# Performance work log

Hardware: AMD Instinct MI355X
Metric: run time of the kernel (lower is better)

## Reference

```python
import jax, jax.numpy as jnp
import numpy as np

N_EMBD = 1024
N_HEAD = 16
HEAD = N_EMBD // N_HEAD
D_FF = 4 * N_EMBD
B, T = 2, 2048


def setup_inputs() -> dict:
    key = jax.random.key(0)
    ks = jax.random.split(key, 12)
    s = 0.02
    return {
        "x": jax.random.normal(ks[0], (B, T, N_EMBD), jnp.float32),
        "Wq": jax.random.normal(ks[1], (N_EMBD, N_EMBD), jnp.float32) * s,
        "bq": jnp.zeros((N_EMBD,), jnp.float32),
        "Wk": jax.random.normal(ks[2], (N_EMBD, N_EMBD), jnp.float32) * s,
        "bk": jnp.zeros((N_EMBD,), jnp.float32),
        "Wv": jax.random.normal(ks[3], (N_EMBD, N_EMBD), jnp.float32) * s,
        "bv": jnp.zeros((N_EMBD,), jnp.float32),
        "Wo": jax.random.normal(ks[4], (N_EMBD, N_EMBD), jnp.float32) * s,
        "bo": jnp.zeros((N_EMBD,), jnp.float32),
        "W1": jax.random.normal(ks[5], (N_EMBD, D_FF), jnp.float32) * s,
        "b1": jnp.zeros((D_FF,), jnp.float32),
        "W2": jax.random.normal(ks[6], (D_FF, N_EMBD), jnp.float32) * s,
        "b2": jnp.zeros((N_EMBD,), jnp.float32),
        "g1": jnp.ones((N_EMBD,), jnp.float32),
        "be1": jnp.zeros((N_EMBD,), jnp.float32),
        "g2": jnp.ones((N_EMBD,), jnp.float32),
        "be2": jnp.zeros((N_EMBD,), jnp.float32),
    }


def _layernorm(x, g, b, eps=1e-3):
    # keras LayerNormalization default epsilon=1e-3
    mu = jnp.mean(x, axis=-1, keepdims=True)
    var = jnp.mean(jnp.square(x - mu), axis=-1, keepdims=True)
    return (x - mu) * jax.lax.rsqrt(var + eps) * g + b


def _attention(h, Wq, bq, Wk, bk, Wv, bv, Wo, bo):
    b, t, _ = h.shape
    q = (h @ Wq + bq).reshape(b, t, N_HEAD, HEAD)
    k = (h @ Wk + bk).reshape(b, t, N_HEAD, HEAD)
    v = (h @ Wv + bv).reshape(b, t, N_HEAD, HEAD)
    scores = jnp.einsum("bthd,bshd->bhts", q, k) / jnp.sqrt(jnp.float32(HEAD))
    causal = jnp.tril(jnp.ones((t, t), bool))
    scores = jnp.where(causal, scores, -jnp.inf)
    w = jax.nn.softmax(scores, axis=-1)  # dropout is identity in eval
    ctx = jnp.einsum("bhts,bshd->bthd", w, v).reshape(b, t, N_EMBD)
    return ctx @ Wo + bo


def reference(x, Wq, bq, Wk, bk, Wv, bv, Wo, bo, W1, b1, W2, b2, g1, be1, g2, be2):
    x = x + _attention(_layernorm(x, g1, be1), Wq, bq, Wk, bk, Wv, bv, Wo, bo)
    h = _layernorm(x, g2, be2)
    ff = jax.nn.relu(h @ W1 + b1) @ W2 + b2
    return x + ff
```

## Files before the change

### kernel.cpp

```cpp
#include <hip/hip_runtime.h>

typedef __bf16 bf16;
typedef __attribute__((ext_vector_type(8))) __bf16 bf16x8;
typedef __attribute__((ext_vector_type(4))) __bf16 bf16x4;
typedef __attribute__((ext_vector_type(4))) float f32x4;

#define MFMA16(A, B, C) __builtin_amdgcn_mfma_f32_16x16x32_bf16(A, B, C, 0, 0, 0)

#define GLOAD16(gp, lp)                                          \
  __builtin_amdgcn_global_load_lds(                              \
      (const __attribute__((address_space(1))) void*)(gp),       \
      (__attribute__((address_space(3))) void*)(lp), 16, 0, 0)

__device__ __forceinline__ float fexp2(float x) {
#if __has_builtin(__builtin_amdgcn_exp2f)
  return __builtin_amdgcn_exp2f(x);
#else
  float r;
  asm("v_exp_f32 %0, %1" : "=v"(r) : "v"(x));
  return r;
#endif
}

#define QSCL 0.18033688011112042f

__global__ __launch_bounds__(256) void transpose_cvt_kernel(
    const float* __restrict__ in, bf16* __restrict__ out, int K, int N)
{
  __shared__ float tile[32][33];
  const int kt = blockIdx.y * 32;
  const int nt = blockIdx.x * 32;
  const int tx = threadIdx.x, ty = threadIdx.y;
#pragma unroll
  for (int j = 0; j < 4; ++j)
    tile[ty + j * 8][tx] = in[(size_t)(kt + ty + j * 8) * N + nt + tx];
  __syncthreads();
#pragma unroll
  for (int j = 0; j < 4; ++j)
    out[(size_t)(nt + ty + j * 8) * K + kt + tx] = (bf16)tile[tx][ty + j * 8];
}

__global__ __launch_bounds__(256) void transpose4_cvt_kernel(
    const float* __restrict__ w0, const float* __restrict__ w1,
    const float* __restrict__ w2, const float* __restrict__ w3,
    bf16* __restrict__ out)
{
  __shared__ float tile[32][33];
  const float* srcs[4] = {w0, w1, w2, w3};
  const float* in = srcs[blockIdx.z];
  bf16* o = out + (size_t)blockIdx.z * 1024 * 1024;
  const int kt = blockIdx.y * 32;
  const int nt = blockIdx.x * 32;
  const int tx = threadIdx.x, ty = threadIdx.y;
#pragma unroll
  for (int j = 0; j < 4; ++j)
    tile[ty + j * 8][tx] = in[(size_t)(kt + ty + j * 8) * 1024 + nt + tx];
  __syncthreads();
#pragma unroll
  for (int j = 0; j < 4; ++j)
    o[(size_t)(nt + ty + j * 8) * 1024 + kt + tx] = (bf16)tile[tx][ty + j * 8];
}

__global__ __launch_bounds__(256) void ln_kernel(
    const float* __restrict__ in, const float* __restrict__ gamma,
    const float* __restrict__ beta, bf16* __restrict__ out)
{
  const int row = blockIdx.x;
  const int t = threadIdx.x;
  const float4 v = ((const float4*)(in + (size_t)row * 1024))[t];
  float s = v.x + v.y + v.z + v.w;
  float sq = v.x * v.x + v.y * v.y + v.z * v.z + v.w * v.w;
#pragma unroll
  for (int m = 1; m < 64; m <<= 1) {
    s += __shfl_xor(s, m);
    sq += __shfl_xor(sq, m);
  }
  __shared__ float ssum[4], ssq[4];
  const int w = t >> 6;
  if ((t & 63) == 0) { ssum[w] = s; ssq[w] = sq; }
  __syncthreads();
  s = ssum[0] + ssum[1] + ssum[2] + ssum[3];
  sq = ssq[0] + ssq[1] + ssq[2] + ssq[3];
  const float mu = s * (1.0f / 1024.0f);
  const float var = sq * (1.0f / 1024.0f) - mu * mu;
  const float rs = rsqrtf(var + 1e-3f);
  const float4 g = ((const float4*)gamma)[t];
  const float4 b = ((const float4*)beta)[t];
  bf16x4 o;
  o[0] = (bf16)((v.x - mu) * rs * g.x + b.x);
  o[1] = (bf16)((v.y - mu) * rs * g.y + b.y);
  o[2] = (bf16)((v.z - mu) * rs * g.z + b.z);
  o[3] = (bf16)((v.w - mu) * rs * g.w + b.w);
  *(bf16x4*)(out + (size_t)row * 1024 + t * 4) = o;
}

__global__ __launch_bounds__(256) void ln_b_kernel(
    const bf16* __restrict__ in, const float* __restrict__ gamma,
    const float* __restrict__ beta, bf16* __restrict__ out)
{
  const int row = blockIdx.x;
  const int t = threadIdx.x;
  const bf16x4 vb = *(const bf16x4*)(in + (size_t)row * 1024 + t * 4);
  float v0 = (float)vb[0], v1 = (float)vb[1], v2 = (float)vb[2], v3 = (float)vb[3];
  float s = v0 + v1 + v2 + v3;
  float sq = v0 * v0 + v1 * v1 + v2 * v2 + v3 * v3;
#pragma unroll
  for (int m = 1; m < 64; m <<= 1) {
    s += __shfl_xor(s, m);
    sq += __shfl_xor(sq, m);
  }
  __shared__ float ssum[4], ssq[4];
  const int w = t >> 6;
  if ((t & 63) == 0) { ssum[w] = s; ssq[w] = sq; }
  __syncthreads();
  s = ssum[0] + ssum[1] + ssum[2] + ssum[3];
  sq = ssq[0] + ssq[1] + ssq[2] + ssq[3];
  const float mu = s * (1.0f / 1024.0f);
  const float var = sq * (1.0f / 1024.0f) - mu * mu;
  const float rs = rsqrtf(var + 1e-3f);
  const float4 g = ((const float4*)gamma)[t];
  const float4 b = ((const float4*)beta)[t];
  bf16x4 o;
  o[0] = (bf16)((v0 - mu) * rs * g.x + b.x);
  o[1] = (bf16)((v1 - mu) * rs * g.y + b.y);
  o[2] = (bf16)((v2 - mu) * rs * g.z + b.z);
  o[3] = (bf16)((v3 - mu) * rs * g.w + b.w);
  *(bf16x4*)(out + (size_t)row * 1024 + t * 4) = o;
}

template <int BM, int BN, int BK, int EPI, int SWZ>
__global__ __launch_bounds__(256, 2) void gemm_bt(
    const bf16* __restrict__ A, const bf16* __restrict__ Bt,
    const float* __restrict__ bias0, const float* __restrict__ bias1,
    const float* __restrict__ bias2, const float* __restrict__ resid,
    const bf16* __restrict__ residb,
    bf16* __restrict__ out0, bf16* __restrict__ out1, bf16* __restrict__ out2,
    float* __restrict__ outf, int M, int N, int K)
{
  constexpr int WM = BM / 2, WN = BN / 2;
  constexpr int MI = WM / 16, NJ = WN / 16;
  constexpr int KK = BK / 32;
  constexpr int NSLOT = BK / 8;
  constexpr int SMASK = NSLOT - 1;
  constexpr int RPL = 512 / BK;
  constexpr int ALOADS = BM / (4 * RPL);
  constexpr int BLOADS = BN / (4 * RPL);
  constexpr int S = ALOADS + BLOADS;

  __shared__ bf16 As[3][BM * BK];
  __shared__ bf16 Bs[3][BN * BK];
  const int tid = threadIdx.x;
  const int lane = tid & 63, w = tid >> 6;
  const int wr = w >> 1, wc = w & 1;
  const int g = lane >> 4, lr = lane & 15;

  int bx = blockIdx.x, by = blockIdx.y;
  if constexpr (SWZ) {
    const int bid = bx + gridDim.x * by;
    const int xcd = bid & 7, idx = bid >> 3;
    const int chunk = gridDim.y >> 3;
    by = xcd * chunk + (idx % chunk);
    bx = idx / chunk;
  }
  const int brow = by * BM, bcol = bx * BN;

  f32x4 acc[MI][NJ] = {};

  const int lrow = lane / NSLOT;
  const int slot = lane & SMASK;
  int lcol;
  if constexpr (BK == 32)
    lcol = ((slot - (lrow >> 1)) & 3) * 8;
  else
    lcol = (slot ^ (lrow & 7)) * 8;

  auto stage = [&](int buf, int k0) {
#pragma unroll
    for (int j = 0; j < ALOADS; ++j) {
      const int row0 = w * (BM / 4) + j * RPL;
      GLOAD16(A + (size_t)(brow + row0 + lrow) * K + k0 + lcol,
              &As[buf][row0 * BK]);
    }
#pragma unroll
    for (int j = 0; j < BLOADS; ++j) {
      const int row0 = w * (BN / 4) + j * RPL;
      GLOAD16(Bt + (size_t)(bcol + row0 + lrow) * K + k0 + lcol,
              &Bs[buf][row0 * BK]);
    }
  };

  auto rdslot = [&](int kg) {
    if constexpr (BK == 32) return ((kg + (lr >> 1)) & 3) * 8;
    else return (kg ^ (lr & 7)) * 8;
  };

  const int nk = K / BK;
  stage(0, 0);
  stage(1, BK);
  int cur = 0;
  for (int t = 0; t < nk; ++t) {
    if (t + 1 < nk) {
      if constexpr (S == 3)
        asm volatile("s_waitcnt vmcnt(3)" ::: "memory");
      else if constexpr (S == 4)
        asm volatile("s_waitcnt vmcnt(4)" ::: "memory");
      else
        asm volatile("s_waitcnt vmcnt(6)" ::: "memory");
    } else {
      asm volatile("s_waitcnt vmcnt(0)" ::: "memory");
    }
    __builtin_amdgcn_s_barrier();
    __builtin_amdgcn_sched_barrier(0);

    bf16x8 afr[MI][KK], bfr[NJ][KK];
#pragma unroll
    for (int i = 0; i < MI; ++i)
#pragma unroll
      for (int kk = 0; kk < KK; ++kk)
        afr[i][kk] = *(const bf16x8*)&As[cur][(wr * WM + i * 16 + lr) * BK +
                                             rdslot(kk * 4 + g)];
#pragma unroll
    for (int j = 0; j < NJ; ++j)
#pragma unroll
      for (int kk = 0; kk < KK; ++kk)
        bfr[j][kk] = *(const bf16x8*)&Bs[cur][(wc * WN + j * 16 + lr) * BK +
                                             rdslot(kk * 4 + g)];

    if (t + 2 < nk) {
      int nb = cur + 2;
      if (nb >= 3) nb -= 3;
      stage(nb, (t + 2) * BK);
    }

    __builtin_amdgcn_s_setprio(1);
#pragma unroll
    for (int kk = 0; kk < KK; ++kk)
#pragma unroll
      for (int i = 0; i < MI; ++i)
#pragma unroll
        for (int j = 0; j < NJ; ++j)
          acc[i][j] = MFMA16(afr[i][kk], bfr[j][kk], acc[i][j]);
    __builtin_amdgcn_s_setprio(0);

    ++cur;
    if (cur == 3) cur = 0;
  }

#pragma unroll
  for (int i = 0; i < MI; ++i) {
#pragma unroll
    for (int j = 0; j < NJ; ++j) {
      const int r0 = brow + wr * WM + i * 16 + g * 4;
      const int c = bcol + wc * WN + j * 16 + lr;
      if constexpr (EPI == 1) {
        const float bv = bias0[c];
#pragma unroll
        for (int rr = 0; rr < 4; ++rr)
          out0[(size_t)(r0 + rr) * N + c] =
              (bf16)fmaxf(acc[i][j][rr] + bv, 0.0f);
      } else if constexpr (EPI == 5) {
        const float bv = bias0[c];
#pragma unroll
        for (int rr = 0; rr < 4; ++rr) {
          const size_t idx = (size_t)(r0 + rr) * N + c;
          out0[idx] = (bf16)(acc[i][j][rr] + bv + resid[idx]);
        }
      } else if constexpr (EPI == 6) {
        const float bv = bias0[c];
#pragma unroll
        for (int rr = 0; rr < 4; ++rr) {
          const size_t idx = (size_t)(r0 + rr) * N + c;
          outf[idx] = acc[i][j][rr] + bv + (float)residb[idx];
        }
      } else {
        const int sub = c >> 10;
        const int c1 = c & 1023;
        if (sub == 0) {
          const float bv = bias0[c1];
#pragma unroll
          for (int rr = 0; rr < 4; ++rr)
            out0[(size_t)(r0 + rr) * 1024 + c1] =
                (bf16)((acc[i][j][rr] + bv) * QSCL);
        } else if (sub == 1) {
          const float bv = bias1[c1];
#pragma unroll
          for (int rr = 0; rr < 4; ++rr)
            out1[(size_t)(r0 + rr) * 1024 + c1] = (bf16)(acc[i][j][rr] + bv);
        } else {
          const float bv = bias2[c1];
          const int bb = r0 >> 11, t0 = r0 & 2047;
          const int hh = c1 >> 6, dd = c1 & 63;
          bf16x4 pk;
#pragma unroll
          for (int rr = 0; rr < 4; ++rr) pk[rr] = (bf16)(acc[i][j][rr] + bv);
          *(bf16x4*)(out2 + ((size_t)((bb * 16 + hh) * 64 + dd)) * 2048 + t0) = pk;
        }
      }
    }
  }
}

__global__ __launch_bounds__(256) void attn_kernel(
    const bf16* __restrict__ q, const bf16* __restrict__ kmat,
    const bf16* __restrict__ vt, bf16* __restrict__ ctx)
{
  __shared__ bf16 Ks[64 * 64];
  __shared__ bf16 Vs[64 * 64];
  __shared__ bf16 Pq[4][16][88];
  const int bx = blockIdx.x, by = blockIdx.y;
  const int k4 = by >> 3;
  const int qt = (k4 == 0) ? bx
               : (k4 == 1) ? (31 - bx)
               : (k4 == 2) ? (bx ^ 16)
                           : (31 - (bx ^ 16));
  const int b_ = by >> 4, h_ = by & 15;
  const int qb = qt * 64;
  const int tid = threadIdx.x;
  const int lane = tid & 63, w = tid >> 6;
  const int g = lane >> 4, lr = lane & 15;
  const int qrow = qb + w * 16 + lr;

  bf16x8 qf[2];
  {
    const bf16* qp = q + (size_t)(b_ * 2048 + qrow) * 1024 + h_ * 64 + g * 8;
    qf[0] = *(const bf16x8*)qp;
    qf[1] = *(const bf16x8*)(qp + 32);
  }

  f32x4 o[4] = {};
  float l = 0.f;

  const int srow = tid >> 2;
  const int c16 = (tid & 3) * 16;
  const int rb = srow * 128;
  const int sw = (srow & 7) << 4;
  const bf16* kbase = kmat + (size_t)(b_ * 2048) * 1024 + h_ * 64;
  const bf16* vbase = vt + (size_t)(b_ * 16 + h_) * 64 * 2048;
  const bf16* kp0 = kbase + (size_t)srow * 1024 + c16;
  const bf16* vp0 = vbase + (size_t)srow * 2048 + c16;

  bf16x8 k0 = *(const bf16x8*)kp0;
  bf16x8 k1 = *(const bf16x8*)(kp0 + 8);
  bf16x8 v0 = *(const bf16x8*)vp0;
  bf16x8 v1 = *(const bf16x8*)(vp0 + 8);

  for (int s0 = 0; s0 <= qb; s0 += 64) {
    *(bf16x8*)((char*)Ks + ((rb + c16 * 2) ^ sw)) = k0;
    *(bf16x8*)((char*)Ks + ((rb + c16 * 2 + 16) ^ sw)) = k1;
    *(bf16x8*)((char*)Vs + ((rb + c16 * 2) ^ sw)) = v0;
    *(bf16x8*)((char*)Vs + ((rb + c16 * 2 + 16) ^ sw)) = v1;
    __syncthreads();
    if (s0 < qb) {
      const bf16* kp = kp0 + (size_t)(s0 + 64) * 1024;
      k0 = *(const bf16x8*)kp;
      k1 = *(const bf16x8*)(kp + 8);
      const bf16* vp = vp0 + (s0 + 64);
      v0 = *(const bf16x8*)vp;
      v1 = *(const bf16x8*)(vp + 8);
    }

    f32x4 st[4];
    __builtin_amdgcn_s_setprio(1);
#pragma unroll
    for (int n = 0; n < 4; ++n) {
      f32x4 z = {};
#pragma unroll
      for (int kk = 0; kk < 2; ++kk) {
        const int row = n * 16 + lr;
        bf16x8 ak = *(const bf16x8*)((char*)Ks +
            ((row * 128 + kk * 64 + g * 16) ^ ((lr & 7) << 4)));
        z = MFMA16(ak, qf[kk], z);
      }
      st[n] = z;
    }
    __builtin_amdgcn_s_setprio(0);

    if (s0 == qb) {
#pragma unroll
      for (int n = 0; n < 4; ++n)
#pragma unroll
        for (int r = 0; r < 4; ++r)
          if (s0 + n * 16 + g * 4 + r > qrow) st[n][r] = -1e30f;
    }

    float rs = 0.f;
#pragma unroll
    for (int n = 0; n < 4; ++n) {
      bf16x4 pk;
#pragma unroll
      for (int r = 0; r < 4; ++r) {
        const float p = fexp2(st[n][r]);
        rs += p;
        pk[r] = (bf16)p;
      }
      *(bf16x4*)&Pq[w][lr][n * 16 + g * 4] = pk;
    }

    bf16x8 pa[2];
#pragma unroll
    for (int kk = 0; kk < 2; ++kk)
      pa[kk] = *(const bf16x8*)&Pq[w][lr][kk * 32 + g * 8];
    __builtin_amdgcn_s_setprio(1);
#pragma unroll
    for (int n = 0; n < 4; ++n) {
      const int row = n * 16 + lr;
#pragma unroll
      for (int kk = 0; kk < 2; ++kk) {
        bf16x8 bv = *(const bf16x8*)((char*)Vs +
            ((row * 128 + kk * 64 + g * 16) ^ ((lr & 7) << 4)));
        o[n] = MFMA16(pa[kk], bv, o[n]);
      }
    }
    __builtin_amdgcn_s_setprio(0);

    rs += __shfl_xor(rs, 16);
    rs += __shfl_xor(rs, 32);
    l += rs;
    __syncthreads();
  }

  float lq[4];
#pragma unroll
  for (int r = 0; r < 4; ++r) lq[r] = __shfl(l, g * 4 + r);
#pragma unroll
  for (int r = 0; r < 4; ++r) {
    const float inv = 1.0f / lq[r];
#pragma unroll
    for (int n = 0; n < 4; ++n)
      ctx[(size_t)(b_ * 2048 + qb + w * 16 + g * 4 + r) * 1024 + h_ * 64 + n * 16 + lr] =
          (bf16)(o[n][r] * inv);
  }
}

extern "C" void kernel_launch(void* const* d_in, const int* in_sizes, int n_in,
                              void* d_out, int out_size, void* d_ws, size_t ws_size,
                              hipStream_t stream)
{
  (void)in_sizes; (void)n_in; (void)out_size; (void)ws_size;
  const float* x   = (const float*)d_in[0];
  const float* Wq  = (const float*)d_in[1];
  const float* bq  = (const float*)d_in[2];
  const float* Wk  = (const float*)d_in[3];
  const float* bk  = (const float*)d_in[4];
  const float* Wv  = (const float*)d_in[5];
  const float* bv  = (const float*)d_in[6];
  const float* Wo  = (const float*)d_in[7];
  const float* bo  = (const float*)d_in[8];
  const float* W1  = (const float*)d_in[9];
  const float* b1  = (const float*)d_in[10];
  const float* W2  = (const float*)d_in[11];
  const float* b2  = (const float*)d_in[12];
  const float* g1  = (const float*)d_in[13];
  const float* be1 = (const float*)d_in[14];
  const float* g2  = (const float*)d_in[15];
  const float* be2 = (const float*)d_in[16];
  float* out = (float*)d_out;

  char* ws = (char*)d_ws;
  const size_t MB = 1024 * 1024;
  bf16* wqkv_t = (bf16*)(ws + 0 * MB);
  bf16* wo_t = (bf16*)(ws + 6 * MB);
  bf16* w1_t = (bf16*)(ws + 8 * MB);
  bf16* w2_t = (bf16*)(ws + 16 * MB);
  bf16* h1   = (bf16*)(ws + 24 * MB);
  bf16* qbuf = (bf16*)(ws + 32 * MB);
  bf16* kbuf = (bf16*)(ws + 40 * MB);
  bf16* vtb  = (bf16*)(ws + 48 * MB);
  bf16* ctx  = (bf16*)(ws + 56 * MB);
  bf16* h2   = (bf16*)(ws + 64 * MB);
  bf16* x2b  = (bf16*)(ws + 72 * MB);
  bf16* ff1  = (bf16*)(ws + 24 * MB);

  const dim3 tb(32, 8);
  transpose4_cvt_kernel<<<dim3(32, 32, 4), tb, 0, stream>>>(
      Wq, Wk, Wv, Wo, wqkv_t);
  transpose_cvt_kernel<<<dim3(128, 32), tb, 0, stream>>>(W1, w1_t, 1024, 4096);
  transpose_cvt_kernel<<<dim3(32, 128), tb, 0, stream>>>(W2, w2_t, 4096, 1024);

  ln_kernel<<<4096, 256, 0, stream>>>(x, g1, be1, h1);

  gemm_bt<128, 128, 32, 4, 0><<<dim3(24, 32), 256, 0, stream>>>(
      h1, wqkv_t, bq, bk, bv, nullptr, nullptr, qbuf, kbuf, vtb, nullptr,
      4096, 3072, 1024);

  attn_kernel<<<dim3(32, 32), 256, 0, stream>>>(qbuf, kbuf, vtb, ctx);

  gemm_bt<128, 64, 64, 5, 0><<<dim3(16, 32), 256, 0, stream>>>(
      ctx, wo_t, bo, nullptr, nullptr, x, nullptr, x2b, nullptr, nullptr,
      nullptr, 4096, 1024, 1024);

  ln_b_kernel<<<4096, 256, 0, stream>>>(x2b, g2, be2, h2);

  gemm_bt<256, 128, 32, 1, 0><<<dim3(32, 16), 256, 0, stream>>>(
      h2, w1_t, b1, nullptr, nullptr, nullptr, nullptr, ff1, nullptr, nullptr,
      nullptr, 4096, 4096, 1024);

  gemm_bt<128, 64, 64, 6, 1><<<dim3(16, 32), 256, 0, stream>>>(
      ff1, w2_t, b2, nullptr, nullptr, nullptr, x2b, nullptr, nullptr, nullptr,
      out, 4096, 1024, 4096);
}
```

Before: 199.8 us.

## Process 128 keys per attention iteration with double K/V shared tiles

The causal attention loop now stages 128 keys per iteration into two 64-row K and V shared-memory sub-tiles. It then runs the QK, exp and PV steps on each half before the next barrier. This halves the number of block-wide synchronisations and issues larger, wider global prefetches per thread to hide load latency. The cost is a doubled shared-memory footprint and more registers. When the query tile index is even, the final iteration computes a fully masked 64-key half, which is wasted work.

New measurement: 214.0 us. +7.1%, slower.

```diff
diff --git a/kernel.cpp b/kernel.cpp
--- a/kernel.cpp
+++ b/kernel.cpp
@@ -304,8 +304,8 @@
     const bf16* __restrict__ q, const bf16* __restrict__ kmat,
     const bf16* __restrict__ vt, bf16* __restrict__ ctx)
 {
-  __shared__ bf16 Ks[64 * 64];
-  __shared__ bf16 Vs[64 * 64];
+  __shared__ bf16 Ks[2][64 * 64];
+  __shared__ bf16 Vs[2][64 * 64];
   __shared__ bf16 Pq[4][16][88];
   const int bx = blockIdx.x, by = blockIdx.y;
   const int k4 = by >> 3;
@@ -330,36 +330,46 @@
   f32x4 o[4] = {};
   float l = 0.f;
 
-  const int srow = tid >> 2;
-  const int c16 = (tid & 3) * 16;
-  const int rb = srow * 128;
-  const int sw = (srow & 7) << 4;
+  const int sKloc = tid >> 1;
+  const int ksub = sKloc >> 6, kr64 = sKloc & 63;
+  const int kc = (tid & 1) * 32;
+  const int ksw = (kr64 & 7) << 4;
+  const int vrow = tid >> 2;
+  const int vcol = (tid & 3) * 32;
+  const int vsub = vcol >> 6, vs64 = vcol & 63;
+  const int vsw = (vrow & 7) << 4;
+
   const bf16* kbase = kmat + (size_t)(b_ * 2048) * 1024 + h_ * 64;
   const bf16* vbase = vt + (size_t)(b_ * 16 + h_) * 64 * 2048;
-  const bf16* kp0 = kbase + (size_t)srow * 1024 + c16;
-  const bf16* vp0 = vbase + (size_t)srow * 2048 + c16;
-
-  bf16x8 k0 = *(const bf16x8*)kp0;
-  bf16x8 k1 = *(const bf16x8*)(kp0 + 8);
-  bf16x8 v0 = *(const bf16x8*)vp0;
-  bf16x8 v1 = *(const bf16x8*)(vp0 + 8);
-
-  for (int s0 = 0; s0 <= qb; s0 += 64) {
-    *(bf16x8*)((char*)Ks + ((rb + c16 * 2) ^ sw)) = k0;
-    *(bf16x8*)((char*)Ks + ((rb + c16 * 2 + 16) ^ sw)) = k1;
-    *(bf16x8*)((char*)Vs + ((rb + c16 * 2) ^ sw)) = v0;
-    *(bf16x8*)((char*)Vs + ((rb + c16 * 2 + 16) ^ sw)) = v1;
+
+  bf16x8 kr[4], vr[4];
+  auto ldKV = [&](int s0) {
+    const bf16* kp = kbase + (size_t)(s0 + sKloc) * 1024 + kc;
+    kr[0] = *(const bf16x8*)(kp);
+    kr[1] = *(const bf16x8*)(kp + 8);
+    kr[2] = *(const bf16x8*)(kp + 16);
+    kr[3] = *(const bf16x8*)(kp + 24);
+    const bf16* vp = vbase + (size_t)vrow * 2048 + s0 + vcol;
+    vr[0] = *(const bf16x8*)(vp);
+    vr[1] = *(const bf16x8*)(vp + 8);
+    vr[2] = *(const bf16x8*)(vp + 16);
+    vr[3] = *(const bf16x8*)(vp + 24);
+  };
+
+  const int ns = (qt >> 1) + 1;
+  ldKV(0);
+
+  for (int t = 0; t < ns; ++t) {
+    const int s0 = t << 7;
+#pragma unroll
+    for (int j = 0; j < 4; ++j) {
+      *(bf16x8*)((char*)Ks[ksub] + ((kr64 * 128 + kc * 2 + j * 16) ^ ksw)) = kr[j];
+      *(bf16x8*)((char*)Vs[vsub] + ((vrow * 128 + vs64 * 2 + j * 16) ^ vsw)) = vr[j];
+    }
     __syncthreads();
-    if (s0 < qb) {
-      const bf16* kp = kp0 + (size_t)(s0 + 64) * 1024;
-      k0 = *(const bf16x8*)kp;
-      k1 = *(const bf16x8*)(kp + 8);
-      const bf16* vp = vp0 + (s0 + 64);
-      v0 = *(const bf16x8*)vp;
-      v1 = *(const bf16x8*)(vp + 8);
-    }
-
-    f32x4 st[4];
+    if (t + 1 < ns) ldKV(s0 + 128);
+
+    f32x4 st0[4], st1[4];
     __builtin_amdgcn_s_setprio(1);
 #pragma unroll
     for (int n = 0; n < 4; ++n) {
@@ -367,20 +377,34 @@
 #pragma unroll
       for (int kk = 0; kk < 2; ++kk) {
         const int row = n * 16 + lr;
-        bf16x8 ak = *(const bf16x8*)((char*)Ks +
+        bf16x8 ak = *(const bf16x8*)((char*)Ks[0] +
             ((row * 128 + kk * 64 + g * 16) ^ ((lr & 7) << 4)));
         z = MFMA16(ak, qf[kk], z);
       }
-      st[n] = z;
+      st0[n] = z;
+    }
+#pragma unroll
+    for (int n = 0; n < 4; ++n) {
+      f32x4 z = {};
+#pragma unroll
+      for (int kk = 0; kk < 2; ++kk) {
+        const int row = n * 16 + lr;
+        bf16x8 ak = *(const bf16x8*)((char*)Ks[1] +
+            ((row * 128 + kk * 64 + g * 16) ^ ((lr & 7) << 4)));
+        z = MFMA16(ak, qf[kk], z);
+      }
+      st1[n] = z;
     }
     __builtin_amdgcn_s_setprio(0);
 
-    if (s0 == qb) {
+    if (t == ns - 1) {
 #pragma unroll
       for (int n = 0; n < 4; ++n)
 #pragma unroll
-        for (int r = 0; r < 4; ++r)
-          if (s0 + n * 16 + g * 4 + r > qrow) st[n][r] = -1e30f;
+        for (int r = 0; r < 4; ++r) {
+          if (s0 + n * 16 + g * 4 + r > qrow) st0[n][r] = -1e30f;
+          if (s0 + 64 + n * 16 + g * 4 + r > qrow) st1[n][r] = -1e30f;
+        }
     }
 
     float rs = 0.f;
@@ -389,29 +413,59 @@
       bf16x4 pk;
 #pragma unroll
       for (int r = 0; r < 4; ++r) {
-        const float p = fexp2(st[n][r]);
+        const float p = fexp2(st0[n][r]);
         rs += p;
         pk[r] = (bf16)p;
       }
       *(bf16x4*)&Pq[w][lr][n * 16 + g * 4] = pk;
     }
-
-    bf16x8 pa[2];
-#pragma unroll
-    for (int kk = 0; kk < 2; ++kk)
-      pa[kk] = *(const bf16x8*)&Pq[w][lr][kk * 32 + g * 8];
-    __builtin_amdgcn_s_setprio(1);
+    {
+      bf16x8 pa[2];
+#pragma unroll
+      for (int kk = 0; kk < 2; ++kk)
+        pa[kk] = *(const bf16x8*)&Pq[w][lr][kk * 32 + g * 8];
+      __builtin_amdgcn_s_setprio(1);
+#pragma unroll
+      for (int n = 0; n < 4; ++n) {
+        const int row = n * 16 + lr;
+#pragma unroll
+        for (int kk = 0; kk < 2; ++kk) {
+          bf16x8 bv = *(const bf16x8*)((char*)Vs[0] +
+              ((row * 128 + kk * 64 + g * 16) ^ ((lr & 7) << 4)));
+          o[n] = MFMA16(pa[kk], bv, o[n]);
+        }
+      }
+      __builtin_amdgcn_s_setprio(0);
+    }
 #pragma unroll
     for (int n = 0; n < 4; ++n) {
-      const int row = n * 16 + lr;
-#pragma unroll
-      for (int kk = 0; kk < 2; ++kk) {
-        bf16x8 bv = *(const bf16x8*)((char*)Vs +
-            ((row * 128 + kk * 64 + g * 16) ^ ((lr & 7) << 4)));
-        o[n] = MFMA16(pa[kk], bv, o[n]);
-      }
-    }
-    __builtin_amdgcn_s_setprio(0);
+      bf16x4 pk;
+#pragma unroll
+      for (int r = 0; r < 4; ++r) {
+        const float p = fexp2(st1[n][r]);
+        rs += p;
+        pk[r] = (bf16)p;
+      }
+      *(bf16x4*)&Pq[w][lr][n * 16 + g * 4] = pk;
+    }
+    {
+      bf16x8 pa[2];
+#pragma unroll
+      for (int kk = 0; kk < 2; ++kk)
+        pa[kk] = *(const bf16x8*)&Pq[w][lr][kk * 32 + g * 8];
+      __builtin_amdgcn_s_setprio(1);
+#pragma unroll
+      for (int n = 0; n < 4; ++n) {
+        const int row = n * 16 + lr;
+#pragma unroll
+        for (int kk = 0; kk < 2; ++kk) {
+          bf16x8 bv = *(const bf16x8*)((char*)Vs[1] +
+              ((row * 128 + kk * 64 + g * 16) ^ ((lr & 7) << 4)));
+          o[n] = MFMA16(pa[kk], bv, o[n]);
+        }
+      }
+      __builtin_amdgcn_s_setprio(0);
+    }
 
     rs += __shfl_xor(rs, 16);
     rs += __shfl_xor(rs, 32);
```
